# Kernel optimization log

Hardware: AMD Instinct MI355X
Metric: run time of the kernel (lower is better)

The kernel has to match this reference:

```python
import jax, jax.numpy as jnp
import numpy as np

NUM = 5          # spline intervals
KS = 3           # spline order k
GRID_LO, GRID_HI = -1.0, 1.0
KH = KW = 3      # kernel size
STRIDE = 1
PAD = 1
DIL = 1


def make_grid():
    # extended uniform grid: num+2k+1 points from lo-k*h to hi+k*h (h=(hi-lo)/num)
    h = (GRID_HI - GRID_LO) / NUM
    return GRID_LO + jnp.arange(-KS, NUM + KS + 1, dtype=jnp.float32) * h  # (12,)


def b_spline_basis(x, grid, k):
    # x: (..., ), grid: (G,) shared across features (all rows of pykan grid identical)
    # returns (..., G-1-k) Cox-de Boor bases of order k
    x = x[..., None]
    B = ((x >= grid[:-1]) & (x < grid[1:])).astype(x.dtype)
    for p in range(1, k + 1):
        left = (x - grid[:-(p + 1)]) / (grid[p:-1] - grid[:-(p + 1)]) * B[..., :-1]
        right = (grid[p + 1:] - x) / (grid[p + 1:] - grid[1:-p]) * B[..., 1:]
        B = left + right
    return B


def extract_patches(x):
    # torch.nn.Unfold ordering: (B, C, kh*kw, OH, OW), kernel positions row-major
    x = jnp.pad(x, ((0, 0), (0, 0), (PAD, PAD), (PAD, PAD)))
    B, C, H, W = x.shape
    OH = (H - DIL * (KH - 1) - 1) // STRIDE + 1
    OW = (W - DIL * (KW - 1) - 1) // STRIDE + 1
    pats = []
    for i in range(KH):
        for j in range(KW):
            pats.append(x[:, :, i * DIL:i * DIL + STRIDE * (OH - 1) + 1:STRIDE,
                          j * DIL:j * DIL + STRIDE * (OW - 1) + 1:STRIDE])
    return jnp.stack(pats, axis=2)  # (B, C, K, OH, OW)


def setup_inputs() -> dict:
    key = jax.random.key(0)
    k1, k2, k3, k4, k5 = jax.random.split(key, 5)
    B, C, O, H, W = 8, 32, 64, 32, 32
    K, M = KH * KW, NUM + KS
    x = jax.random.normal(k1, (B, C, H, W), dtype=jnp.float32)
    coef = jax.random.normal(k2, (O, C, K, M), dtype=jnp.float32) * 0.1
    scale_base = jax.random.normal(k3, (O, C, K), dtype=jnp.float32) / np.sqrt(K)
    scale_sp = jnp.ones((O, C, K), dtype=jnp.float32)
    bias = jnp.zeros((O,), dtype=jnp.float32)
    return {"x": x, "coef": coef, "scale_base": scale_base,
            "scale_sp": scale_sp, "bias": bias}


def reference(x, coef, scale_base, scale_sp, bias):
    grid = make_grid()
    p = extract_patches(x)                              # (B, C, K, OH, OW)
    B, C, K, OH, OW = p.shape
    t = p.transpose(0, 1, 3, 4, 2).reshape(B, C, OH * OW, K)  # (B, C, L, K)
    Bsp = b_spline_basis(t, grid, KS)                   # (B, C, L, K, M)
    silu = t * jax.nn.sigmoid(t)
    W_sp = scale_sp[..., None] * coef                   # (O, C, K, M)
    out = (jnp.einsum('bclk,ock->bol', silu, scale_base)
           + jnp.einsum('bclkm,ockm->bol', Bsp, W_sp))
    out = out + bias[None, :, None]
    return out.reshape(B, -1, OH, OW)
```

## Files before the change

kernel.cpp:

```cpp
#include <hip/hip_runtime.h>


typedef __attribute__((ext_vector_type(8))) short v8s;
typedef __attribute__((ext_vector_type(4))) float v4f;
typedef __attribute__((ext_vector_type(4))) int   v4i;
typedef unsigned short ushort_t;

#define CELL_STRIDE 296
#define ROW_STRIDE  (34 * CELL_STRIDE)

__device__ __forceinline__ unsigned short f2bf(float v) {
  union { float f; unsigned int u; } w; w.f = v;
  unsigned int r = w.u + 0x7FFFu + ((w.u >> 16) & 1u);
  return (unsigned short)(r >> 16);
}

__global__ __launch_bounds__(256) void kan_prep(const float* __restrict__ coef,
                                                const float* __restrict__ sb,
                                                const float* __restrict__ ssp,
                                                ushort_t* __restrict__ Wb) {
  __shared__ ushort_t row_[2592];
  const int o   = blockIdx.x;
  const int tid = threadIdx.x;
  const float* cf   = coef + o * 2304;
  const float* sspo = ssp  + o * 288;
  const float* sbo  = sb   + o * 288;

#pragma unroll
  for (int k = 0; k < 9; ++k) {
    int l   = k * 256 + tid;
    int c   = l / 72;
    int rem = l - c * 72;
    int pos = rem >> 3;
    int m   = rem & 7;
    float v = sspo[c * 9 + pos] * cf[l];
    row_[(pos * 9 + m + 1) * 32 + c] = f2bf(v);
  }
  for (int t = tid; t < 288; t += 256) {
    int c = t / 9, pos = t - c * 9;
    row_[(pos * 9) * 32 + c] = f2bf(sbo[t]);
  }
  __syncthreads();
  unsigned int* dst = (unsigned int*)(Wb + (size_t)o * 2592);
  const unsigned int* src = (const unsigned int*)row_;
  for (int i = tid; i < 1296; i += 256) dst[i] = src[i];
}

template <int LO, int HI>
__device__ __forceinline__ void kloop(const ushort_t* __restrict__ fb,
                                      const ushort_t* __restrict__ wp,
                                      v4f& acc0, v4f& acc1) {
#pragma unroll
  for (int s = LO; s < HI; ++s) {
    const int di = s / 27;
    const int dj = (s / 9) % 3;
    const int kk = s % 9;
    const int fo = di * ROW_STRIDE + dj * CELL_STRIDE + kk * 32;
    v8s wf = *(const v8s*)(wp + s * 32);
    v8s a0 = *(const v8s*)(fb + fo);
    v8s a1 = *(const v8s*)(fb + fo + 16 * CELL_STRIDE);
    acc0 = __builtin_amdgcn_mfma_f32_16x16x32_bf16(wf, a0, acc0, 0, 0, 0);
    acc1 = __builtin_amdgcn_mfma_f32_16x16x32_bf16(wf, a1, acc1, 0, 0, 0);
  }
}

__global__ __launch_bounds__(1024, 4) void kan_fused(const float* __restrict__ x,
                                                     const ushort_t* __restrict__ Wb,
                                                     const float* __restrict__ bias,
                                                     float* __restrict__ out) {
  __shared__ __align__(16) ushort_t feat[3 * ROW_STRIDE];
  __shared__ float xs[32 * 33];
  __shared__ ushort_t dump[64];

  const int tid = threadIdx.x;
  const int bx  = blockIdx.x;
  const int oh  = bx & 31;
  const int b   = bx >> 5;

  {
    v4i z = {0, 0, 0, 0};
    v4i* fz = (v4i*)feat;
#pragma unroll
    for (int k = 0; k < 4; ++k) {
      int i = tid + k * 1024;
      if (i < 3774) fz[i] = z;
    }
  }

  for (int r = 0; r < 3; ++r) {
    const int h = oh + r - 1;
    const bool hval = (h >= 0) && (h < 32);
    if (hval) {
      int c = tid >> 5, w = tid & 31;
      xs[c * 33 + w] = x[(((b * 32 + c) * 32 + h) * 32 + w)];
    }
    __syncthreads();
    for (int idx = tid; idx < 1088; idx += 1024) {
      int c = idx & 31, cell = idx >> 5;
      int wi = cell - 1;
      float t = 0.0f;
      if (hval && wi >= 0 && wi < 32) t = xs[c * 33 + wi];

      unsigned short f0 = f2bf(t / (1.0f + __expf(-t)));
      float u  = (t + 2.2f) * 2.5f;
      float fi = floorf(u);
      int   i  = (int)fi;
      float s  = u - fi;
      float s2 = s * s, s3 = s2 * s;
      float om = 1.0f - s;
      float w0 = om * om * om * (1.0f / 6.0f);
      float w1 = (4.0f - 6.0f * s2 + 3.0f * s3) * (1.0f / 6.0f);
      float w2 = (1.0f + 3.0f * s + 3.0f * s2 - 3.0f * s3) * (1.0f / 6.0f);
      float w3 = s3 * (1.0f / 6.0f);

      ushort_t* cb = feat + r * ROW_STRIDE + cell * CELL_STRIDE + c;
      cb[0] = f0;
#pragma unroll
      for (int d = 0; d < 4; ++d) {
        float wv_ = (d == 0) ? w0 : (d == 1) ? w1 : (d == 2) ? w2 : w3;
        int jj = i - 3 + d;
        ushort_t* p = ((unsigned)jj <= 7u) ? (cb + (jj + 1) * 32)
                                           : (dump + (tid & 63));
        *p = f2bf(wv_);
      }
    }
    __syncthreads();
  }

  const int wv   = tid >> 6;
  const int lane = tid & 63;
  const int row  = lane & 15;
  const int quad = lane >> 4;
  const int og   = wv & 3;
  const int kq   = wv >> 2;
  const int obase = og * 16;

  const ushort_t* fb = feat + row * CELL_STRIDE + quad * 8;
  const ushort_t* wp = Wb + (size_t)(obase + row) * 2592 + quad * 8;

  v4f acc0 = {0.f, 0.f, 0.f, 0.f};
  v4f acc1 = acc0;

  if (kq == 0)      kloop<0, 20>(fb, wp, acc0, acc1);
  else if (kq == 1) kloop<20, 40>(fb, wp, acc0, acc1);
  else if (kq == 2) kloop<40, 60>(fb, wp, acc0, acc1);
  else              kloop<60, 81>(fb, wp, acc0, acc1);

  __syncthreads();
  float* red = (float*)feat;
  if (kq != 0) {
    float* rp = red + ((kq - 1) * 4 + og) * 512 + quad * 4 * 32 + row;
#pragma unroll
    for (int r = 0; r < 4; ++r) {
      rp[r * 32]      = acc0[r];
      rp[r * 32 + 16] = acc1[r];
    }
  }
  __syncthreads();
  if (kq == 0) {
    float* o0 = out + ((size_t)(b * 64 + obase + quad * 4)) * 1024 + oh * 32 + row;
#pragma unroll
    for (int r = 0; r < 4; ++r) {
      float bv = bias[obase + quad * 4 + r];
      float s0 = acc0[r], s1 = acc1[r];
#pragma unroll
      for (int gs = 0; gs < 3; ++gs) {
        const float* rp = red + (gs * 4 + og) * 512 + (quad * 4 + r) * 32 + row;
        s0 += rp[0];
        s1 += rp[16];
      }
      o0[(size_t)r * 1024]      = s0 + bv;
      o0[(size_t)r * 1024 + 16] = s1 + bv;
    }
  }
}

extern "C" void kernel_launch(void* const* d_in, const int* in_sizes, int n_in,
                              void* d_out, int out_size, void* d_ws, size_t ws_size,
                              hipStream_t stream) {
  const float* x    = (const float*)d_in[0];
  const float* coef = (const float*)d_in[1];
  const float* sb   = (const float*)d_in[2];
  const float* ssp  = (const float*)d_in[3];
  const float* bias = (const float*)d_in[4];
  float* out = (float*)d_out;

  ushort_t* Wb = (ushort_t*)d_ws;

  hipLaunchKernelGGL(kan_prep, dim3(64), dim3(256), 0, stream, coef, sb, ssp, Wb);
  hipLaunchKernelGGL(kan_fused, dim3(256), dim3(1024), 0, stream, x, Wb, bias, out);
}
```

Before: 75.22 us.

## Widen per-wave output tile to 32 channels, split K eight ways, batch input loads

```diff
diff --git a/kernel.cpp b/kernel.cpp
--- a/kernel.cpp
+++ b/kernel.cpp
@@ -8,6 +8,10 @@
 
 #define CELL_STRIDE 296
 #define ROW_STRIDE  (34 * CELL_STRIDE)
+#define FEAT_BYTES  (3 * ROW_STRIDE * 2)
+#define XS_OFF      FEAT_BYTES
+#define DUMP_OFF    (XS_OFF + 12672)
+#define SMEM_BYTES  (DUMP_OFF + 128)
 
 __device__ __forceinline__ unsigned short f2bf(float v) {
   union { float f; unsigned int u; } w; w.f = v;
@@ -47,20 +51,23 @@
 }
 
 template <int LO, int HI>
-__device__ __forceinline__ void kloop(const ushort_t* __restrict__ fb,
-                                      const ushort_t* __restrict__ wp,
-                                      v4f& acc0, v4f& acc1) {
+__device__ __forceinline__ void kloop2(const ushort_t* __restrict__ fb,
+                                       const ushort_t* __restrict__ wp0,
+                                       v4f& a00, v4f& a01, v4f& a10, v4f& a11) {
 #pragma unroll
   for (int s = LO; s < HI; ++s) {
     const int di = s / 27;
     const int dj = (s / 9) % 3;
     const int kk = s % 9;
     const int fo = di * ROW_STRIDE + dj * CELL_STRIDE + kk * 32;
-    v8s wf = *(const v8s*)(wp + s * 32);
+    v8s w0 = *(const v8s*)(wp0 + s * 32);
+    v8s w1 = *(const v8s*)(wp0 + 16 * 2592 + s * 32);
     v8s a0 = *(const v8s*)(fb + fo);
     v8s a1 = *(const v8s*)(fb + fo + 16 * CELL_STRIDE);
-    acc0 = __builtin_amdgcn_mfma_f32_16x16x32_bf16(wf, a0, acc0, 0, 0, 0);
-    acc1 = __builtin_amdgcn_mfma_f32_16x16x32_bf16(wf, a1, acc1, 0, 0, 0);
+    a00 = __builtin_amdgcn_mfma_f32_16x16x32_bf16(w0, a0, a00, 0, 0, 0);
+    a01 = __builtin_amdgcn_mfma_f32_16x16x32_bf16(w0, a1, a01, 0, 0, 0);
+    a10 = __builtin_amdgcn_mfma_f32_16x16x32_bf16(w1, a0, a10, 0, 0, 0);
+    a11 = __builtin_amdgcn_mfma_f32_16x16x32_bf16(w1, a1, a11, 0, 0, 0);
   }
 }
 
@@ -68,9 +75,11 @@
                                                      const ushort_t* __restrict__ Wb,
                                                      const float* __restrict__ bias,
                                                      float* __restrict__ out) {
-  __shared__ __align__(16) ushort_t feat[3 * ROW_STRIDE];
-  __shared__ float xs[32 * 33];
-  __shared__ ushort_t dump[64];
+  __shared__ __align__(16) unsigned char smem[SMEM_BYTES];
+  ushort_t* feat = (ushort_t*)smem;
+  float*    xs   = (float*)(smem + XS_OFF);
+  ushort_t* dump = (ushort_t*)(smem + DUMP_OFF);
+  float*    red  = (float*)smem;
 
   const int tid = threadIdx.x;
   const int bx  = blockIdx.x;
@@ -87,19 +96,25 @@
     }
   }
 
+#pragma unroll
+  for (int r = 0; r < 3; ++r) {
+    const int h = oh + r - 1;
+    if (h >= 0 && h < 32) {
+      int c = tid >> 5, w = tid & 31;
+      xs[r * 1056 + c * 33 + w] = x[(((b * 32 + c) * 32 + h) * 32 + w)];
+    }
+  }
+  __syncthreads();
+
+#pragma unroll
   for (int r = 0; r < 3; ++r) {
     const int h = oh + r - 1;
     const bool hval = (h >= 0) && (h < 32);
-    if (hval) {
-      int c = tid >> 5, w = tid & 31;
-      xs[c * 33 + w] = x[(((b * 32 + c) * 32 + h) * 32 + w)];
-    }
-    __syncthreads();
     for (int idx = tid; idx < 1088; idx += 1024) {
       int c = idx & 31, cell = idx >> 5;
       int wi = cell - 1;
       float t = 0.0f;
-      if (hval && wi >= 0 && wi < 32) t = xs[c * 33 + wi];
+      if (hval && wi >= 0 && wi < 32) t = xs[r * 1056 + c * 33 + wi];
 
       unsigned short f0 = f2bf(t / (1.0f + __expf(-t)));
       float u  = (t + 2.2f) * 2.5f;
@@ -124,54 +139,57 @@
         *p = f2bf(wv_);
       }
     }
-    __syncthreads();
-  }
+  }
+  __syncthreads();
 
   const int wv   = tid >> 6;
   const int lane = tid & 63;
   const int row  = lane & 15;
   const int quad = lane >> 4;
-  const int og   = wv & 3;
-  const int kq   = wv >> 2;
-  const int obase = og * 16;
-
-  const ushort_t* fb = feat + row * CELL_STRIDE + quad * 8;
-  const ushort_t* wp = Wb + (size_t)(obase + row) * 2592 + quad * 8;
-
-  v4f acc0 = {0.f, 0.f, 0.f, 0.f};
-  v4f acc1 = acc0;
-
-  if (kq == 0)      kloop<0, 20>(fb, wp, acc0, acc1);
-  else if (kq == 1) kloop<20, 40>(fb, wp, acc0, acc1);
-  else if (kq == 2) kloop<40, 60>(fb, wp, acc0, acc1);
-  else              kloop<60, 81>(fb, wp, acc0, acc1);
-
-  __syncthreads();
-  float* red = (float*)feat;
-  if (kq != 0) {
-    float* rp = red + ((kq - 1) * 4 + og) * 512 + quad * 4 * 32 + row;
+  const int og   = wv & 1;
+  const int kq   = wv >> 1;
+  const int obase = og * 32;
+
+  const ushort_t* fb  = feat + row * CELL_STRIDE + quad * 8;
+  const ushort_t* wp0 = Wb + (size_t)(obase + row) * 2592 + quad * 8;
+
+  v4f a00 = {0.f, 0.f, 0.f, 0.f};
+  v4f a01 = a00, a10 = a00, a11 = a00;
+
+  if      (kq == 0) kloop2< 0, 11>(fb, wp0, a00, a01, a10, a11);
+  else if (kq == 1) kloop2<11, 21>(fb, wp0, a00, a01, a10, a11);
+  else if (kq == 2) kloop2<21, 31>(fb, wp0, a00, a01, a10, a11);
+  else if (kq == 3) kloop2<31, 41>(fb, wp0, a00, a01, a10, a11);
+  else if (kq == 4) kloop2<41, 51>(fb, wp0, a00, a01, a10, a11);
+  else if (kq == 5) kloop2<51, 61>(fb, wp0, a00, a01, a10, a11);
+  else if (kq == 6) kloop2<61, 71>(fb, wp0, a00, a01, a10, a11);
+  else              kloop2<71, 81>(fb, wp0, a00, a01, a10, a11);
+
+  __syncthreads();
+  {
+    float* rp = red + kq * 2112 + (obase + quad * 4) * 33 + row;
 #pragma unroll
     for (int r = 0; r < 4; ++r) {
-      rp[r * 32]      = acc0[r];
-      rp[r * 32 + 16] = acc1[r];
-    }
-  }
-  __syncthreads();
-  if (kq == 0) {
-    float* o0 = out + ((size_t)(b * 64 + obase + quad * 4)) * 1024 + oh * 32 + row;
-#pragma unroll
-    for (int r = 0; r < 4; ++r) {
-      float bv = bias[obase + quad * 4 + r];
-      float s0 = acc0[r], s1 = acc1[r];
-#pragma unroll
-      for (int gs = 0; gs < 3; ++gs) {
-        const float* rp = red + (gs * 4 + og) * 512 + (quad * 4 + r) * 32 + row;
-        s0 += rp[0];
-        s1 += rp[16];
-      }
-      o0[(size_t)r * 1024]      = s0 + bv;
-      o0[(size_t)r * 1024 + 16] = s1 + bv;
-    }
+      rp[r * 33]       = a00[r];
+      rp[r * 33 + 16]  = a01[r];
+      rp[r * 33 + 528] = a10[r];
+      rp[r * 33 + 544] = a11[r];
+    }
+  }
+  __syncthreads();
+  {
+    int o  = tid >> 4;
+    int p0 = (tid & 15) * 2;
+    float s0 = 0.f, s1 = 0.f;
+#pragma unroll
+    for (int g = 0; g < 8; ++g) {
+      const float* rp = red + g * 2112 + o * 33 + p0;
+      s0 += rp[0];
+      s1 += rp[1];
+    }
+    float bv = bias[o];
+    float2 v; v.x = s0 + bv; v.y = s1 + bv;
+    *(float2*)(out + ((size_t)(b * 64 + o)) * 1024 + oh * 32 + p0) = v;
   }
 }
 
```

Result: no change. 75.51 us (+0.4%).
